# Performance work log

Hardware: AMD Instinct MI355X
Metric: run time of the kernel (lower is better)

The kernel has to match this reference:

```python
import jax, jax.numpy as jnp
import numpy as np

IN_F, OUT_F, RANK, ALPHA = 4096, 4096, 8, 32.0

def setup_inputs() -> dict:
    key = jax.random.key(0)
    kx, kw, ka, kb, kbias = jax.random.split(key, 5)
    x = jax.random.normal(kx, (4, 2048, IN_F), dtype=jnp.float32)
    weight = jax.random.normal(kw, (OUT_F, IN_F), dtype=jnp.float32) * 0.02
    a = jax.random.normal(ka, (OUT_F, RANK), dtype=jnp.float32) * 0.02
    b = jax.random.normal(kb, (RANK, IN_F), dtype=jnp.float32) * 0.02  # zeros in init; use randn for nontrivial test
    bias = jax.random.normal(kbias, (OUT_F,), dtype=jnp.float32) * 0.02
    return {"x": x, "weight": weight, "a": a, "b": b, "bias": bias}

def reference(x, weight, a, b, bias):
    # F.linear(x, W, bias) + F.linear(x, a @ b) * alpha / r
    base = jnp.einsum('bsi,oi->bso', x, weight) + bias
    # low-rank path computed in factored form (same math as x @ (a@b).T)
    lora = jnp.einsum('bsr,or->bso', jnp.einsum('bsi,ri->bsr', x, b), a)
    return base + lora * (ALPHA / RANK)
```

## Files before the change

### kernel.cpp

```cpp
#include <hip/hip_runtime.h>
#include <stdint.h>

#define IN_F 4096
#define OUT_F 4096
#define M_TOT 8192
#define LORA_SCALE 4.0f

typedef unsigned short u16;
typedef __attribute__((ext_vector_type(8))) short bf16x8;
typedef __attribute__((ext_vector_type(4))) float f32x4;

__device__ __forceinline__ u16 f2bf(float f) {
  union { float f; unsigned u; } v; v.f = f;
  unsigned r = v.u + 0x7FFFu + ((v.u >> 16) & 1u);
  return (u16)(r >> 16);
}

__device__ __forceinline__ void gload_lds16(const void* g, void* l) {
  __builtin_amdgcn_global_load_lds(
      (const __attribute__((address_space(1))) void*)g,
      (__attribute__((address_space(3))) void*)l, 16, 0, 0);
}

__global__ void prep(const float* __restrict__ X, const float* __restrict__ W,
                     const float* __restrict__ A, const float* __restrict__ B,
                     u16* __restrict__ Xb, u16* __restrict__ Wb) {
  int bid = blockIdx.x;
  if (bid < 16384) {
    size_t base = ((size_t)bid * blockDim.x + threadIdx.x) * 8;
    const f32x4* p = (const f32x4*)(X + base);
    f32x4 v0 = __builtin_nontemporal_load(p);
    f32x4 v1 = __builtin_nontemporal_load(p + 1);
    uint4 pk;
    pk.x = (unsigned)f2bf(v0.x) | ((unsigned)f2bf(v0.y) << 16);
    pk.y = (unsigned)f2bf(v0.z) | ((unsigned)f2bf(v0.w) << 16);
    pk.z = (unsigned)f2bf(v1.x) | ((unsigned)f2bf(v1.y) << 16);
    pk.w = (unsigned)f2bf(v1.z) | ((unsigned)f2bf(v1.w) << 16);
    *(uint4*)(Xb + base) = pk;
  } else {
    int idx = (bid - 16384) * blockDim.x + threadIdx.x;
    int o  = idx >> 10;
    int i0 = (idx & 1023) << 2;
    const f32x4 w = __builtin_nontemporal_load((const f32x4*)(W + (size_t)o * IN_F + i0));
    float a0 = w.x, a1 = w.y, a2 = w.z, a3 = w.w;
#pragma unroll
    for (int r = 0; r < 8; ++r) {
      float ar = A[o * 8 + r] * LORA_SCALE;
      const float4 bv = *(const float4*)(B + (size_t)r * IN_F + i0);
      a0 += ar * bv.x; a1 += ar * bv.y; a2 += ar * bv.z; a3 += ar * bv.w;
    }
    uint2 pk;
    pk.x = (unsigned)f2bf(a0) | ((unsigned)f2bf(a1) << 16);
    pk.y = (unsigned)f2bf(a2) | ((unsigned)f2bf(a3) << 16);
    *(uint2*)(Wb + (size_t)o * IN_F + i0) = pk;
  }
}


#define ABASE(b) ((b) * 32768)
#define BBASE(b) ((b) * 32768 + 16384)

#define STAGE_A(b, h, kt) do { \
  gload_lds16(aG + (size_t)((h) * 128) * IN_F + (kt),      lds + ABASE(b) + ((h) * 128) * 64      + tid * 8); \
  gload_lds16(aG + (size_t)((h) * 128 + 64) * IN_F + (kt), lds + ABASE(b) + ((h) * 128 + 64) * 64 + tid * 8); \
} while (0)

#define STAGE_B(b, h, kt) do { \
  gload_lds16(bG + (size_t)((h) * 128) * IN_F + (kt),      lds + BBASE(b) + ((h) * 128) * 64      + tid * 8); \
  gload_lds16(bG + (size_t)((h) * 128 + 64) * IN_F + (kt), lds + BBASE(b) + ((h) * 128 + 64) * 64 + tid * 8); \
} while (0)

#define WAIT4 asm volatile("s_waitcnt vmcnt(4)" ::: "memory")
#define WAIT0 asm volatile("s_waitcnt vmcnt(0)" ::: "memory")

#define MFMA16 __builtin_amdgcn_mfma_f32_16x16x32_bf16

#define KHALF(b, s, TAIL_STAGE) do { \
  __builtin_amdgcn_s_barrier(); \
  __builtin_amdgcn_sched_barrier(0); \
  _Pragma("unroll") \
  for (int n = 0; n < 4; ++n) \
    Bf[n] = *(const bf16x8*)(lds + BBASE(b) + (rB + n * 16) * 64 + ((s) ? ck1 : ck0)); \
  _Pragma("unroll") \
  for (int m = 0; m < 8; ++m) \
    Af[m] = *(const bf16x8*)(lds + ABASE(b) + (rA + m * 16) * 64 + ((s) ? ck1 : ck0)); \
  __builtin_amdgcn_s_setprio(1); \
  _Pragma("unroll") \
  for (int m = 0; m < 8; ++m) \
    _Pragma("unroll") \
    for (int n = 0; n < 4; ++n) \
      acc[m][n] = MFMA16(Af[m], Bf[n], acc[m][n], 0, 0, 0); \
  __builtin_amdgcn_s_setprio(0); \
  TAIL_STAGE; \
} while (0)

__global__ __launch_bounds__(512, 2) void gemm8(const u16* __restrict__ Xb,
                                                const u16* __restrict__ Wb,
                                                const float* __restrict__ bias,
                                                float* __restrict__ out) {
  extern __shared__ u16 lds[];

  const int tid  = threadIdx.x;
  const int lane = tid & 63;
  const int wid  = tid >> 6;
  const int wr = wid >> 2, wc = wid & 3;
  const int lr = lane & 15, kg = lane >> 4;

  const int bid = blockIdx.x;
  const int swz = (bid & 7) * 64 + (bid >> 3);
  const int mt = swz >> 4, nt = swz & 15;
  const int m0 = mt * 256, n0 = nt * 256;

  const int srow = tid >> 3;
  const int swc  = (tid & 7) ^ (srow & 7);
  const u16* aG = Xb + (size_t)(m0 + srow) * IN_F + swc * 8;
  const u16* bG = Wb + (size_t)(n0 + srow) * IN_F + swc * 8;

  const int rA = wr * 128 + lr;
  const int rB = wc * 64 + lr;
  const int ck0 = ((kg) ^ (lane & 7)) * 8;
  const int ck1 = ((4 + kg) ^ (lane & 7)) * 8;

  f32x4 acc[8][4] = {};
  bf16x8 Af[8], Bf[4];

  STAGE_B(0, 0, 0); STAGE_B(0, 1, 0);
  STAGE_A(0, 0, 0); STAGE_A(0, 1, 0);
  STAGE_B(1, 0, 64); STAGE_B(1, 1, 64);
  WAIT4;

  for (int i = 0; i < 31; ++i) {
    const int kt1 = i * 128 + 64, kt2 = i * 128 + 128, kt3 = i * 128 + 192;
    KHALF(0, 0, STAGE_A(1, 0, kt1); STAGE_A(1, 1, kt1));
    KHALF(0, 1, STAGE_B(0, 0, kt2); STAGE_B(0, 1, kt2));
    WAIT4;
    KHALF(1, 0, STAGE_A(0, 0, kt2); STAGE_A(0, 1, kt2));
    KHALF(1, 1, STAGE_B(1, 0, kt3); STAGE_B(1, 1, kt3));
    WAIT4;
  }
  KHALF(0, 0, STAGE_A(1, 0, 4032); STAGE_A(1, 1, 4032));
  KHALF(0, 1, );
  WAIT0;
  KHALF(1, 0, );
  KHALF(1, 1, );

  float bv[4];
#pragma unroll
  for (int n = 0; n < 4; ++n) bv[n] = bias[n0 + wc * 64 + n * 16 + lr];
  const int rbase = m0 + wr * 128 + kg * 4;
#pragma unroll
  for (int m = 0; m < 8; ++m)
#pragma unroll
    for (int n = 0; n < 4; ++n) {
      int col = n0 + wc * 64 + n * 16 + lr;
#pragma unroll
      for (int r = 0; r < 4; ++r)
        __builtin_nontemporal_store(acc[m][n][r] + bv[n],
                                    &out[(size_t)(rbase + m * 16 + r) * OUT_F + col]);
    }
}

__global__ __launch_bounds__(256) void gemm_bias(const u16* __restrict__ Xb,
                                                 const u16* __restrict__ Wb,
                                                 const float* __restrict__ bias,
                                                 float* __restrict__ out) {
  __shared__ __align__(16) u16 ldsA[128 * 64];
  __shared__ __align__(16) u16 ldsB[128 * 64];

  const int tid  = threadIdx.x;
  const int wid  = tid >> 6;
  const int lane = tid & 63;
  const int nt = blockIdx.x & 31;
  const int mt = blockIdx.x >> 5;
  const int m0 = mt * 128, n0 = nt * 128;
  const int wr = wid >> 1, wc = wid & 1;
  const int lr = lane & 15;
  const int kg = lane >> 4;

  const int srow   = wid * 8 + (lane >> 3);
  const int schunk = (lane & 7) ^ (srow & 7);
  const u16* aSrc = Xb + (size_t)(m0 + srow) * IN_F + schunk * 8;
  const u16* bSrc = Wb + (size_t)(n0 + srow) * IN_F + schunk * 8;

  f32x4 acc[4][4] = {};

  for (int kt = 0; kt < IN_F; kt += 64) {
    __syncthreads();
#pragma unroll
    for (int j = 0; j < 4; ++j) {
      gload_lds16(aSrc + (size_t)(j * 32) * IN_F + kt, &ldsA[j * 2048 + wid * 512]);
      gload_lds16(bSrc + (size_t)(j * 32) * IN_F + kt, &ldsB[j * 2048 + wid * 512]);
    }
    __syncthreads();

#pragma unroll
    for (int s = 0; s < 2; ++s) {
      bf16x8 af[4], bfr[4];
#pragma unroll
      for (int m = 0; m < 4; ++m) {
        int r = wr * 64 + m * 16 + lr;
        int c = (s * 4 + kg) ^ (r & 7);
        af[m] = *(const bf16x8*)&ldsA[r * 64 + c * 8];
      }
#pragma unroll
      for (int n = 0; n < 4; ++n) {
        int r = wc * 64 + n * 16 + lr;
        int c = (s * 4 + kg) ^ (r & 7);
        bfr[n] = *(const bf16x8*)&ldsB[r * 64 + c * 8];
      }
#pragma unroll
      for (int m = 0; m < 4; ++m)
#pragma unroll
        for (int n = 0; n < 4; ++n)
          acc[m][n] = __builtin_amdgcn_mfma_f32_16x16x32_bf16(af[m], bfr[n], acc[m][n], 0, 0, 0);
    }
  }

  float bv[4];
#pragma unroll
  for (int n = 0; n < 4; ++n) bv[n] = bias[n0 + wc * 64 + n * 16 + lr];
  const int rbase = m0 + wr * 64 + kg * 4;
#pragma unroll
  for (int m = 0; m < 4; ++m)
#pragma unroll
    for (int n = 0; n < 4; ++n) {
      int col = n0 + wc * 64 + n * 16 + lr;
#pragma unroll
      for (int r = 0; r < 4; ++r)
        out[(size_t)(rbase + m * 16 + r) * OUT_F + col] = acc[m][n][r] + bv[n];
    }
}

__global__ void lora_t(const float* __restrict__ x, const float* __restrict__ B,
                       float* __restrict__ t) {
  int m = blockIdx.x;
  int tid = threadIdx.x, lane = tid & 63;
  float p[8] = {0, 0, 0, 0, 0, 0, 0, 0};
  for (int k = tid; k < IN_F; k += 256) {
    float xv = x[(size_t)m * IN_F + k];
#pragma unroll
    for (int r = 0; r < 8; ++r) p[r] += xv * B[r * IN_F + k];
  }
#pragma unroll
  for (int r = 0; r < 8; ++r) {
    float v = p[r];
    for (int off = 32; off; off >>= 1) v += __shfl_down(v, off);
    if (lane == 0) atomicAdd(&t[m * 8 + r], v);
  }
}

__global__ void fb_gemm(const float* __restrict__ x, const float* __restrict__ W,
                        const float* __restrict__ A, const float* __restrict__ bias,
                        const float* __restrict__ t, float* __restrict__ out) {
  __shared__ float sx[64][17];
  __shared__ float sw[64][17];
  int tx = threadIdx.x, ty = threadIdx.y;
  int tid = ty * 16 + tx;
  int m0 = blockIdx.y * 64, n0 = blockIdx.x * 64;
  float acc[4][4] = {};
  for (int kt = 0; kt < IN_F; kt += 16) {
    __syncthreads();
#pragma unroll
    for (int q = 0; q < 4; ++q) {
      int idx = q * 256 + tid;
      int r = idx >> 4, c = idx & 15;
      sx[r][c] = x[(size_t)(m0 + r) * IN_F + kt + c];
      sw[r][c] = W[(size_t)(n0 + r) * IN_F + kt + c];
    }
    __syncthreads();
#pragma unroll
    for (int k = 0; k < 16; ++k) {
      float xv[4], wv[4];
#pragma unroll
      for (int i = 0; i < 4; ++i) xv[i] = sx[ty * 4 + i][k];
#pragma unroll
      for (int j = 0; j < 4; ++j) wv[j] = sw[tx * 4 + j][k];
#pragma unroll
      for (int i = 0; i < 4; ++i)
#pragma unroll
        for (int j = 0; j < 4; ++j) acc[i][j] += xv[i] * wv[j];
    }
  }
#pragma unroll
  for (int i = 0; i < 4; ++i) {
    int m = m0 + ty * 4 + i;
    float tv[8];
#pragma unroll
    for (int r = 0; r < 8; ++r) tv[r] = t[m * 8 + r];
#pragma unroll
    for (int j = 0; j < 4; ++j) {
      int o = n0 + tx * 4 + j;
      float lora = 0.f;
#pragma unroll
      for (int r = 0; r < 8; ++r) lora += tv[r] * A[o * 8 + r];
      out[(size_t)m * OUT_F + o] = acc[i][j] + bias[o] + LORA_SCALE * lora;
    }
  }
}

extern "C" void kernel_launch(void* const* d_in, const int* in_sizes, int n_in,
                              void* d_out, int out_size, void* d_ws, size_t ws_size,
                              hipStream_t stream) {
  const float* x    = (const float*)d_in[0];
  const float* W    = (const float*)d_in[1];
  const float* A    = (const float*)d_in[2];
  const float* B    = (const float*)d_in[3];
  const float* bias = (const float*)d_in[4];
  float* out = (float*)d_out;

  const size_t xb_elems = (size_t)M_TOT * IN_F;
  const size_t wb_elems = (size_t)OUT_F * IN_F;
  const size_t need = (xb_elems + wb_elems) * sizeof(u16);

  if (ws_size >= need) {
    u16* Xb = (u16*)d_ws;
    u16* Wb = Xb + xb_elems;
    prep<<<32768, 256, 0, stream>>>(x, W, A, B, Xb, Wb);

    hipError_t e = hipFuncSetAttribute((const void*)gemm8,
                                       hipFuncAttributeMaxDynamicSharedMemorySize,
                                       131072);
    bool used8 = false;
    if (e == hipSuccess) {
      gemm8<<<512, 512, 131072, stream>>>(Xb, Wb, bias, out);
      used8 = (hipGetLastError() == hipSuccess);
    }
    if (!used8) {
      gemm_bias<<<(M_TOT / 128) * (OUT_F / 128), 256, 0, stream>>>(Xb, Wb, bias, out);
    }
  } else {
    float* t = (float*)d_ws;
    (void)hipMemsetAsync(t, 0, (size_t)M_TOT * 8 * sizeof(float), stream);
    lora_t<<<M_TOT, 256, 0, stream>>>(x, B, t);
    fb_gemm<<<dim3(OUT_F / 64, M_TOT / 64), dim3(16, 16), 0, stream>>>(x, W, A, bias, t, out);
  }
}
```

Before: 292.6 us.

## Split GEMM block across 16 waves with 64x64 per-wave tiles

Doubles the gemm8 workgroup from 512 to 1024 threads and reorganizes the waves into a 4x4 grid. Each wave now computes a 64x64 output sub-tile instead of 128x64, with half the accumulators and A fragments. Each thread issues one global-to-LDS load per staging step instead of two, so the vmcnt waits drop from 4 to 2. The goal is more resident waves per CU to hide LDS and memory latency. The trade-offs are fewer MFMAs per LDS fragment read, more barrier participants, and a tight register budget under the new launch bounds that could force spills.

```diff
diff --git a/kernel.cpp b/kernel.cpp
--- a/kernel.cpp
+++ b/kernel.cpp
@@ -60,33 +60,29 @@
 #define ABASE(b) ((b) * 32768)
 #define BBASE(b) ((b) * 32768 + 16384)
 
-#define STAGE_A(b, h, kt) do { \
-  gload_lds16(aG + (size_t)((h) * 128) * IN_F + (kt),      lds + ABASE(b) + ((h) * 128) * 64      + tid * 8); \
-  gload_lds16(aG + (size_t)((h) * 128 + 64) * IN_F + (kt), lds + ABASE(b) + ((h) * 128 + 64) * 64 + tid * 8); \
-} while (0)
-
-#define STAGE_B(b, h, kt) do { \
-  gload_lds16(bG + (size_t)((h) * 128) * IN_F + (kt),      lds + BBASE(b) + ((h) * 128) * 64      + tid * 8); \
-  gload_lds16(bG + (size_t)((h) * 128 + 64) * IN_F + (kt), lds + BBASE(b) + ((h) * 128 + 64) * 64 + tid * 8); \
-} while (0)
-
-#define WAIT4 asm volatile("s_waitcnt vmcnt(4)" ::: "memory")
+#define STAGE_A(b, h, kt) \
+  gload_lds16(aG + (size_t)((h) * 128) * IN_F + (kt), lds + ABASE(b) + ((h) * 128) * 64 + tid * 8)
+
+#define STAGE_B(b, h, kt) \
+  gload_lds16(bG + (size_t)((h) * 128) * IN_F + (kt), lds + BBASE(b) + ((h) * 128) * 64 + tid * 8)
+
+#define WAIT2 asm volatile("s_waitcnt vmcnt(2)" ::: "memory")
 #define WAIT0 asm volatile("s_waitcnt vmcnt(0)" ::: "memory")
 
 #define MFMA16 __builtin_amdgcn_mfma_f32_16x16x32_bf16
 
-#define KHALF(b, s, TAIL_STAGE) do { \
+#define KHALF(b, CKX, TAIL_STAGE) do { \
   __builtin_amdgcn_s_barrier(); \
   __builtin_amdgcn_sched_barrier(0); \
   _Pragma("unroll") \
   for (int n = 0; n < 4; ++n) \
-    Bf[n] = *(const bf16x8*)(lds + BBASE(b) + (rB + n * 16) * 64 + ((s) ? ck1 : ck0)); \
+    Bf[n] = *(const bf16x8*)(lds + BBASE(b) + (rB + n * 16) * 64 + (CKX)); \
   _Pragma("unroll") \
-  for (int m = 0; m < 8; ++m) \
-    Af[m] = *(const bf16x8*)(lds + ABASE(b) + (rA + m * 16) * 64 + ((s) ? ck1 : ck0)); \
+  for (int m = 0; m < 4; ++m) \
+    Af[m] = *(const bf16x8*)(lds + ABASE(b) + (rA + m * 16) * 64 + (CKX)); \
   __builtin_amdgcn_s_setprio(1); \
   _Pragma("unroll") \
-  for (int m = 0; m < 8; ++m) \
+  for (int m = 0; m < 4; ++m) \
     _Pragma("unroll") \
     for (int n = 0; n < 4; ++n) \
       acc[m][n] = MFMA16(Af[m], Bf[n], acc[m][n], 0, 0, 0); \
@@ -94,10 +90,10 @@
   TAIL_STAGE; \
 } while (0)
 
-__global__ __launch_bounds__(512, 2) void gemm8(const u16* __restrict__ Xb,
-                                                const u16* __restrict__ Wb,
-                                                const float* __restrict__ bias,
-                                                float* __restrict__ out) {
+__global__ __launch_bounds__(1024, 4) void gemm8(const u16* __restrict__ Xb,
+                                                 const u16* __restrict__ Wb,
+                                                 const float* __restrict__ bias,
+                                                 float* __restrict__ out) {
   extern __shared__ u16 lds[];
 
   const int tid  = threadIdx.x;
@@ -116,40 +112,40 @@
   const u16* aG = Xb + (size_t)(m0 + srow) * IN_F + swc * 8;
   const u16* bG = Wb + (size_t)(n0 + srow) * IN_F + swc * 8;
 
-  const int rA = wr * 128 + lr;
+  const int rA = wr * 64 + lr;
   const int rB = wc * 64 + lr;
   const int ck0 = ((kg) ^ (lane & 7)) * 8;
   const int ck1 = ((4 + kg) ^ (lane & 7)) * 8;
 
-  f32x4 acc[8][4] = {};
-  bf16x8 Af[8], Bf[4];
+  f32x4 acc[4][4] = {};
+  bf16x8 Af[4], Bf[4];
 
   STAGE_B(0, 0, 0); STAGE_B(0, 1, 0);
   STAGE_A(0, 0, 0); STAGE_A(0, 1, 0);
   STAGE_B(1, 0, 64); STAGE_B(1, 1, 64);
-  WAIT4;
+  WAIT2;
 
   for (int i = 0; i < 31; ++i) {
     const int kt1 = i * 128 + 64, kt2 = i * 128 + 128, kt3 = i * 128 + 192;
-    KHALF(0, 0, STAGE_A(1, 0, kt1); STAGE_A(1, 1, kt1));
-    KHALF(0, 1, STAGE_B(0, 0, kt2); STAGE_B(0, 1, kt2));
-    WAIT4;
-    KHALF(1, 0, STAGE_A(0, 0, kt2); STAGE_A(0, 1, kt2));
-    KHALF(1, 1, STAGE_B(1, 0, kt3); STAGE_B(1, 1, kt3));
-    WAIT4;
-  }
-  KHALF(0, 0, STAGE_A(1, 0, 4032); STAGE_A(1, 1, 4032));
-  KHALF(0, 1, );
+    KHALF(0, ck0, STAGE_A(1, 0, kt1); STAGE_A(1, 1, kt1));
+    KHALF(0, ck1, STAGE_B(0, 0, kt2); STAGE_B(0, 1, kt2));
+    WAIT2;
+    KHALF(1, ck0, STAGE_A(0, 0, kt2); STAGE_A(0, 1, kt2));
+    KHALF(1, ck1, STAGE_B(1, 0, kt3); STAGE_B(1, 1, kt3));
+    WAIT2;
+  }
+  KHALF(0, ck0, STAGE_A(1, 0, 4032); STAGE_A(1, 1, 4032));
+  KHALF(0, ck1, );
   WAIT0;
-  KHALF(1, 0, );
-  KHALF(1, 1, );
+  KHALF(1, ck0, );
+  KHALF(1, ck1, );
 
   float bv[4];
 #pragma unroll
   for (int n = 0; n < 4; ++n) bv[n] = bias[n0 + wc * 64 + n * 16 + lr];
-  const int rbase = m0 + wr * 128 + kg * 4;
-#pragma unroll
-  for (int m = 0; m < 8; ++m)
+  const int rbase = m0 + wr * 64 + kg * 4;
+#pragma unroll
+  for (int m = 0; m < 4; ++m)
 #pragma unroll
     for (int n = 0; n < 4; ++n) {
       int col = n0 + wc * 64 + n * 16 + lr;
@@ -322,7 +318,7 @@
                                        131072);
     bool used8 = false;
     if (e == hipSuccess) {
-      gemm8<<<512, 512, 131072, stream>>>(Xb, Wb, bias, out);
+      gemm8<<<512, 1024, 131072, stream>>>(Xb, Wb, bias, out);
       used8 = (hipGetLastError() == hipSuccess);
     }
     if (!used8) {
```

Measured after the change: 294.0 us. Within noise of the previous version (+0.5%).
